# Kernel optimization log

Measured on AMD Instinct MI355X. Metric: run time of the kernel, lower is better.

## Reference

```python
import jax, jax.numpy as jnp
import numpy as np

V = 32000   # vocab_size
E = 400     # EMBEDDING_SIZE
H = 1150    # HIDDEN_SIZE
B = 16      # batch
T = 128     # seq len

# Reference corresponds to model.eval(): LockedDropout and WeightDrop (DropConnect)
# are identity at eval time, so the math is a plain 3-layer LSTM stack with tied
# embedding/output weights. PyTorch LSTM gate order: i, f, g, o.

def _lstm_layer(x_seq, W_ih, W_hh, b_ih, b_hh, hidden):
    # x_seq: (T, B, I); W_ih: (4H', I); W_hh: (4H', H'); biases: (4H',)
    pre = jnp.einsum('tbi,gi->tbg', x_seq, W_ih) + (b_ih + b_hh)  # (T,B,4H')
    h0 = jnp.zeros((x_seq.shape[1], hidden), x_seq.dtype)
    c0 = jnp.zeros_like(h0)

    def step(carry, pre_t):
        h, c = carry
        gates = pre_t + h @ W_hh.T               # (B, 4H')
        i, f, g, o = jnp.split(gates, 4, axis=-1)
        i = jax.nn.sigmoid(i); f = jax.nn.sigmoid(f)
        g = jnp.tanh(g);       o = jax.nn.sigmoid(o)
        c = f * c + i * g
        h = o * jnp.tanh(c)
        return (h, c), h

    (h_T, c_T), ys = jax.lax.scan(step, (h0, c0), pre)
    return ys, h_T, c_T  # ys: (T,B,H')


def setup_inputs() -> dict:
    key = jax.random.key(0)
    ks = jax.random.split(key, 16)
    s = 1.0 / np.sqrt(H)
    u = lambda k, shape: jax.random.uniform(k, shape, jnp.float32, -s, s)
    inp = {
        'emb':   jax.random.uniform(ks[0], (V, E), jnp.float32, -0.1, 0.1),
        'W_ih1': u(ks[1], (4 * H, E)),  'W_hh1': u(ks[2], (4 * H, H)),
        'b_ih1': u(ks[3], (4 * H,)),    'b_hh1': u(ks[4], (4 * H,)),
        'W_ih2': u(ks[5], (4 * H, H)),  'W_hh2': u(ks[6], (4 * H, H)),
        'b_ih2': u(ks[7], (4 * H,)),    'b_hh2': u(ks[8], (4 * H,)),
        'W_ih3': u(ks[9], (4 * E, H)),  'W_hh3': u(ks[10], (4 * E, E)),
        'b_ih3': u(ks[11], (4 * E,)),   'b_hh3': u(ks[12], (4 * E,)),
        'lin_b': u(ks[13], (V,)),
        'x': jax.random.randint(ks[14], (B, T), 0, V, jnp.int32),
    }
    return inp


def reference(emb, W_ih1, W_hh1, b_ih1, b_hh1,
              W_ih2, W_hh2, b_ih2, b_hh2,
              W_ih3, W_hh3, b_ih3, b_hh3,
              lin_b, x):
    xe = emb[x]                       # (B,T,E)
    xs = jnp.transpose(xe, (1, 0, 2)) # (T,B,E)
    xs, h1, c1 = _lstm_layer(xs, W_ih1, W_hh1, b_ih1, b_hh1, H)
    xs, h2, c2 = _lstm_layer(xs, W_ih2, W_hh2, b_ih2, b_hh2, H)
    xs, h3, c3 = _lstm_layer(xs, W_ih3, W_hh3, b_ih3, b_hh3, E)
    xb = jnp.transpose(xs, (1, 0, 2))                 # (B,T,E)
    logits = jnp.einsum('bte,ve->btv', xb, emb) + lin_b  # tied weights
    out = jnp.transpose(logits, (0, 2, 1))            # (B,V,T)
    return out, h1, h2, h3, c1, c2, c3
```

## Files before the change

kernel.cpp:

```cpp
#include <hip/hip_runtime.h>

typedef _Float16 f16;
typedef _Float16 f16x8 __attribute__((ext_vector_type(8)));
typedef float f32x4 __attribute__((ext_vector_type(4)));

#define BB 16
#define TT 128
#define VV 32000
#define EE 400
#define HH 1150
#define MM 2048

#define NWG1 144
#define NWG2 144
#define NWG3 52
#define NSTEPS 130

__device__ __forceinline__ float sigm(float x){ return 1.f/(1.f + __expf(-x)); }
__device__ __forceinline__ float ftanh(float x){ return 2.f/(1.f + __expf(-2.f*x)) - 1.f; }

__device__ __forceinline__ void ld16c(f16x8& d, const f16* p){
    asm volatile("global_load_dwordx4 %0, %1, off sc0 sc1"
                 : "=v"(d) : "v"(p) : "memory");
}
__device__ __forceinline__ void st2c(f16* p, f16 v){
    asm volatile("global_store_short %0, %1, off sc0 sc1"
                 :: "v"(p), "v"(v) : "memory");
}


__global__ void conv_emb(const float* __restrict__ src, f16* __restrict__ dst){
    int v = blockIdx.y;
    int k = blockIdx.x*256 + threadIdx.x;
    if (k >= 416) return;
    float val = (k < EE) ? src[v*EE + k] : 0.f;
    dst[v*416 + k] = (f16)val;
}

__global__ void embed_gather(const float* __restrict__ emb, const int* __restrict__ x,
                             f16* __restrict__ dst){
    int m = blockIdx.y;
    int k = blockIdx.x*256 + threadIdx.x;
    if (k >= 416) return;
    int t = m >> 4, b = m & 15;
    int row = x[b*TT + t];
    float val = (k < EE) ? emb[row*EE + k] : 0.f;
    dst[m*416 + k] = (f16)val;
}

__global__ void conv_w(const float* __restrict__ src, f16* __restrict__ dst,
                       int Hout, int Ksrc, int Kp){
    int n = blockIdx.y;
    int k = blockIdx.x*256 + threadIdx.x;
    if (k >= Kp) return;
    int j = n >> 2, g = n & 3;
    float val = (j < Hout && k < Ksrc) ? src[(g*Hout + j)*Ksrc + k] : 0.f;
    dst[(size_t)n*Kp + k] = (f16)val;
}

__global__ void conv_bias(const float* __restrict__ bi, const float* __restrict__ bh,
                          float* __restrict__ dst, int Hout, int Np){
    int n = blockIdx.x*256 + threadIdx.x;
    if (n >= Np) return;
    int j = n >> 2, g = n & 3;
    dst[n] = (j < Hout) ? (bi[g*Hout + j] + bh[g*Hout + j]) : 0.f;
}

template<int SC>
__global__ __launch_bounds__(256) void gemm16(
    const f16* __restrict__ A, const f16* __restrict__ B,
    const float* __restrict__ bias, float* __restrict__ C,
    int Kp, int Nst)
{
    __shared__ __align__(16) f16 lA[128*32];
    __shared__ __align__(16) f16 lB[128*32];
    const int lane = threadIdx.x & 63;
    const int wid  = threadIdx.x >> 6;
    const int m0 = blockIdx.y * 128, n0 = blockIdx.x * 128;
    f32x4 acc[4][4] = {};
    const int sr = threadIdx.x >> 2;
    const int sc = (threadIdx.x & 3) * 8;
    for (int k0 = 0; k0 < Kp; k0 += 32) {
        __syncthreads();
        *(f16x8*)&lA[ sr      *32 + sc] = *(const f16x8*)&A[(size_t)(m0 + sr     )*Kp + k0 + sc];
        *(f16x8*)&lA[(sr + 64)*32 + sc] = *(const f16x8*)&A[(size_t)(m0 + sr + 64)*Kp + k0 + sc];
        *(f16x8*)&lB[ sr      *32 + sc] = *(const f16x8*)&B[(size_t)(n0 + sr     )*Kp + k0 + sc];
        *(f16x8*)&lB[(sr + 64)*32 + sc] = *(const f16x8*)&B[(size_t)(n0 + sr + 64)*Kp + k0 + sc];
        __syncthreads();
        const int wr = (wid >> 1) * 64, wc = (wid & 1) * 64;
        f16x8 af[4], bf[4];
        #pragma unroll
        for (int i = 0; i < 4; ++i)
            af[i] = *(const f16x8*)&lA[(wr + i*16 + (lane & 15))*32 + (lane >> 4)*8];
        #pragma unroll
        for (int j = 0; j < 4; ++j)
            bf[j] = *(const f16x8*)&lB[(wc + j*16 + (lane & 15))*32 + (lane >> 4)*8];
        #pragma unroll
        for (int i = 0; i < 4; ++i)
            #pragma unroll
            for (int j = 0; j < 4; ++j)
                acc[i][j] = __builtin_amdgcn_mfma_f32_16x16x32_f16(af[i], bf[j], acc[i][j], 0, 0, 0);
    }
    const int wr = (wid >> 1) * 64, wc = (wid & 1) * 64;
    #pragma unroll
    for (int i = 0; i < 4; ++i) {
        #pragma unroll
        for (int j = 0; j < 4; ++j) {
            int gc = n0 + wc + j*16 + (lane & 15);
            float bb = bias[gc];
            #pragma unroll
            for (int r = 0; r < 4; ++r) {
                int gr = m0 + wr + i*16 + (lane >> 4)*4 + r;
                float v = acc[i][j][r] + bb;
                if (SC) C[((size_t)(gr >> 7)*VV + gc)*TT + (gr & 127)] = v;
                else    C[(size_t)gr*Nst + gc] = v;
            }
        }
    }
}


template<int KIH, int KHH, int DELAY>
__device__ __forceinline__ void lstm_role(
    float (&red)[4][16][32], float (&cst)[16][8],
    const float* __restrict__ pre,
    const float* __restrict__ bias,
    const f16* __restrict__ Wih,
    const f16* __restrict__ Whh,
    const f16* __restrict__ xA, const f16* __restrict__ xB,
    f16* __restrict__ hA, f16* __restrict__ hB,
    f16* __restrict__ xs3,
    float* __restrict__ hout, float* __restrict__ cout,
    unsigned* __restrict__ arrive, int bid, int H)
{
    constexpr int HpHH = KHH * 128;
    constexpr int KIHA = (KIH > 0) ? KIH : 1;
    const int lane = threadIdx.x & 63, kw = threadIdx.x >> 6;
    const int n0 = bid * 32;
    const int nwg = gridDim.x;
    if (threadIdx.x < 128) cst[threadIdx.x & 15][threadIdx.x >> 4] = 0.f;
    const int arow = lane & 15, aoff = (lane >> 4) * 8;
    const size_t hofsHH = (size_t)arow * HpHH + kw * (KHH * 32) + aoff;
    const size_t hofsIH = (size_t)arow * 1152 + kw * 288 + aoff;

    const f16* wph0 = Whh + (size_t)(n0 + arow) * HpHH + kw * (KHH * 32) + aoff;
    const f16* wph1 = wph0 + (size_t)16 * HpHH;
    const f16* wpi0 = (KIH > 0) ? (Wih + (size_t)(n0 + arow) * 1152 + kw * 288 + aoff) : nullptr;
    const f16* wpi1 = (KIH > 0) ? (wpi0 + (size_t)16 * 1152) : nullptr;
    f16x8 wh0[KHH], wh1[KHH];
    #pragma unroll
    for (int i = 0; i < KHH; ++i) {
        wh0[i] = *(const f16x8*)(wph0 + i*32);
        wh1[i] = *(const f16x8*)(wph1 + i*32);
    }
    f16x8 wi0[KIHA], wi1[KIHA];
    if constexpr (KIH > 0) {
        #pragma unroll
        for (int i = 0; i < KIH; ++i) {
            wi0[i] = *(const f16x8*)(wpi0 + i*32);
            wi1[i] = *(const f16x8*)(wpi1 + i*32);
        }
    }
    const int b  = threadIdx.x & 15;
    const int jl = threadIdx.x >> 4;
    f32x4 bias4 = {0.f,0.f,0.f,0.f};
    if constexpr (KIH > 0) {
        if (threadIdx.x < 128) bias4 = *(const f32x4*)(bias + n0 + jl*4);
    }
    __syncthreads();

    for (int s = 0; s < NSTEPS; ++s) {
        const int t = s - DELAY;
        if (t >= 0 && t < TT) {
            const f16* hp = ((t & 1) ? hB : hA) + hofsHH;
            f16* hw       =  (t & 1) ? hA : hB;
            f32x4 p4;
            if constexpr (KIH == 0) {
                if (threadIdx.x < 128)
                    p4 = *(const f32x4*)(pre + (size_t)(t*16 + b)*4608 + n0 + jl*4);
            }
            f16x8 xv[KIHA], hv[KHH];
            if constexpr (KIH > 0) {
                const f16* xp = ((t & 1) ? xA : xB) + hofsIH;
                #pragma unroll
                for (int i = 0; i < KIH; ++i) ld16c(xv[i], xp + i*32);
            }
            #pragma unroll
            for (int i = 0; i < KHH; ++i) ld16c(hv[i], hp + i*32);
            asm volatile("s_waitcnt vmcnt(0)" ::: "memory");
            __builtin_amdgcn_sched_barrier(0);

            f32x4 acc0 = {0.f,0.f,0.f,0.f}, acc1 = {0.f,0.f,0.f,0.f};
            if constexpr (KIH > 0) {
                #pragma unroll
                for (int i = 0; i < KIH; ++i) {
                    acc0 = __builtin_amdgcn_mfma_f32_16x16x32_f16(xv[i], wi0[i], acc0, 0, 0, 0);
                    acc1 = __builtin_amdgcn_mfma_f32_16x16x32_f16(xv[i], wi1[i], acc1, 0, 0, 0);
                }
            }
            #pragma unroll
            for (int i = 0; i < KHH; ++i) {
                acc0 = __builtin_amdgcn_mfma_f32_16x16x32_f16(hv[i], wh0[i], acc0, 0, 0, 0);
                acc1 = __builtin_amdgcn_mfma_f32_16x16x32_f16(hv[i], wh1[i], acc1, 0, 0, 0);
            }
            #pragma unroll
            for (int r = 0; r < 4; ++r) {
                red[kw][(lane >> 4)*4 + r][lane & 15]        = acc0[r];
                red[kw][(lane >> 4)*4 + r][16 + (lane & 15)] = acc1[r];
            }
            __syncthreads();
            if (threadIdx.x < 128) {
                const int nb = jl * 4;
                f32x4 base = (KIH > 0) ? bias4 : p4;
                float gi = base[0] + red[0][b][nb+0] + red[1][b][nb+0] + red[2][b][nb+0] + red[3][b][nb+0];
                float gf = base[1] + red[0][b][nb+1] + red[1][b][nb+1] + red[2][b][nb+1] + red[3][b][nb+1];
                float gg = base[2] + red[0][b][nb+2] + red[1][b][nb+2] + red[2][b][nb+2] + red[3][b][nb+2];
                float go = base[3] + red[0][b][nb+3] + red[1][b][nb+3] + red[2][b][nb+3] + red[3][b][nb+3];
                float c = sigm(gf) * cst[b][jl] + sigm(gi) * ftanh(gg);
                float h = sigm(go) * ftanh(c);
                cst[b][jl] = c;
                const int j = (n0 >> 2) + jl;
                st2c(hw + b*HpHH + j, (f16)h);
                if constexpr (DELAY == 2) xs3[(size_t)(b*TT + t)*416 + j] = (f16)h;
                if (t == TT-1 && j < H) { hout[b*H + j] = h; cout[b*H + j] = c; }
                asm volatile("s_waitcnt vmcnt(0)" ::: "memory");
            }
        }
        if (s == NSTEPS-1) break;
        __syncthreads();
        if (threadIdx.x == 0)
            __hip_atomic_store(&arrive[blockIdx.x * 16], (unsigned)(s + 1),
                               __ATOMIC_RELAXED, __HIP_MEMORY_SCOPE_AGENT);
        for (int w = threadIdx.x; w < nwg; w += 256) {
            while (__hip_atomic_load(&arrive[w * 16], __ATOMIC_RELAXED,
                                     __HIP_MEMORY_SCOPE_AGENT) < (unsigned)(s + 1))
                __builtin_amdgcn_s_sleep(1);
        }
        __syncthreads();
    }
}

__global__ __launch_bounds__(256, 2) void lstm_mega(
    const float* __restrict__ pre1,
    const float* __restrict__ bias2, const float* __restrict__ bias3,
    const f16* __restrict__ whh1,
    const f16* __restrict__ wih2, const f16* __restrict__ whh2,
    const f16* __restrict__ wih3, const f16* __restrict__ whh3,
    f16* h1A, f16* h1B, f16* h2A, f16* h2B, f16* h3A, f16* h3B,
    f16* xs3,
    float* h1o, float* c1o, float* h2o, float* c2o, float* h3o, float* c3o,
    unsigned* arrive)
{
    __shared__ float red[4][16][32];
    __shared__ float cst[16][8];
    const int bx = blockIdx.x;
    if (bx < NWG1) {
        lstm_role<0,9,0>(red, cst, pre1, nullptr, nullptr, whh1,
                         nullptr, nullptr, h1A, h1B, nullptr,
                         h1o, c1o, arrive, bx, HH);
    } else if (bx < NWG1 + NWG2) {
        lstm_role<9,9,1>(red, cst, nullptr, bias2, wih2, whh2,
                         h1A, h1B, h2A, h2B, nullptr,
                         h2o, c2o, arrive, bx - NWG1, HH);
    } else {
        lstm_role<9,4,2>(red, cst, nullptr, bias3, wih3, whh3,
                         h2A, h2B, h3A, h3B, xs3,
                         h3o, c3o, arrive, bx - NWG1 - NWG2, EE);
    }
}

extern "C" void kernel_launch(void* const* d_in, const int* in_sizes, int n_in,
                              void* d_out, int out_size, void* d_ws, size_t ws_size,
                              hipStream_t stream)
{
    const float* emb  = (const float*)d_in[0];
    const float* Wih1 = (const float*)d_in[1];
    const float* Whh1 = (const float*)d_in[2];
    const float* bih1 = (const float*)d_in[3];
    const float* bhh1 = (const float*)d_in[4];
    const float* Wih2 = (const float*)d_in[5];
    const float* Whh2 = (const float*)d_in[6];
    const float* bih2 = (const float*)d_in[7];
    const float* bhh2 = (const float*)d_in[8];
    const float* Wih3 = (const float*)d_in[9];
    const float* Whh3 = (const float*)d_in[10];
    const float* bih3 = (const float*)d_in[11];
    const float* bhh3 = (const float*)d_in[12];
    const float* linb = (const float*)d_in[13];
    const int*   x    = (const int*)d_in[14];
    float* out = (float*)d_out;
    char*  ws  = (char*)d_ws;
    char*  outc = (char*)d_out;

    const size_t ARR  = 0;
    const size_t H1A  = 21760;
    const size_t H1B  = H1A + 36864;
    const size_t H2A  = H1B + 36864;
    const size_t H2B  = H2A + 36864;
    const size_t H3A  = H2B + 36864;
    const size_t H3B  = H3A + 16384;
    const size_t ZEND = H3B + 16384;
    size_t off = ZEND;
    auto alloc = [&](size_t bytes){ size_t r = off; off += (bytes + 255) & ~(size_t)255; return r; };
    const size_t EMBBF = alloc((size_t)VV*416*2);
    const size_t XS0   = alloc((size_t)MM*416*2);
    const size_t XS3   = alloc((size_t)MM*416*2);
    const size_t WIH1  = alloc((size_t)4608*416*2);
    const size_t B1    = alloc((size_t)4608*4);
    const size_t B2    = alloc((size_t)4608*4);
    const size_t B3    = alloc((size_t)1664*4);

    f16* emb_bf = (f16*)(ws + EMBBF);
    f16* xs0    = (f16*)(ws + XS0);
    f16* xs3    = (f16*)(ws + XS3);
    f16* wih1p  = (f16*)(ws + WIH1);
    float* bias1 = (float*)(ws + B1);
    float* bias2 = (float*)(ws + B2);
    float* bias3 = (float*)(ws + B3);
    unsigned* arr = (unsigned*)(ws + ARR);

    float* pre1 = out;
    const size_t OW_HH1 = 37748736;
    const size_t OW_IH2 = OW_HH1 + 10616832;
    const size_t OW_HH2 = OW_IH2 + 10616832;
    const size_t OW_IH3 = OW_HH2 + 10616832;
    const size_t OW_HH3 = OW_IH3 + 3833856;
    f16* whh1p = (f16*)(outc + OW_HH1);
    f16* wih2p = (f16*)(outc + OW_IH2);
    f16* whh2p = (f16*)(outc + OW_HH2);
    f16* wih3p = (f16*)(outc + OW_IH3);
    f16* whh3p = (f16*)(outc + OW_HH3);

    float* H1O = out + 65536000;  float* H2O = H1O + 18400;  float* H3O = H2O + 18400;
    float* C1O = H3O + 6400;      float* C2O = C1O + 18400;  float* C3O = C2O + 18400;

    hipMemsetAsync(d_ws, 0, ZEND, stream);

    conv_emb    <<<dim3(2, VV), 256, 0, stream>>>(emb, emb_bf);
    embed_gather<<<dim3(2, MM), 256, 0, stream>>>(emb, x, xs0);

    conv_w   <<<dim3(2, 4608), 256, 0, stream>>>(Wih1, wih1p, HH, EE, 416);
    conv_bias<<<dim3(18),      256, 0, stream>>>(bih1, bhh1, bias1, HH, 4608);
    gemm16<0><<<dim3(36, 16),  256, 0, stream>>>(xs0, wih1p, bias1, pre1, 416, 4608);

    conv_w   <<<dim3(5, 4608), 256, 0, stream>>>(Whh1, whh1p, HH, HH, 1152);
    conv_w   <<<dim3(5, 4608), 256, 0, stream>>>(Wih2, wih2p, HH, HH, 1152);
    conv_w   <<<dim3(5, 4608), 256, 0, stream>>>(Whh2, whh2p, HH, HH, 1152);
    conv_w   <<<dim3(5, 1664), 256, 0, stream>>>(Wih3, wih3p, EE, HH, 1152);
    conv_w   <<<dim3(2, 1664), 256, 0, stream>>>(Whh3, whh3p, EE, EE, 512);
    conv_bias<<<dim3(18),      256, 0, stream>>>(bih2, bhh2, bias2, HH, 4608);
    conv_bias<<<dim3(7),       256, 0, stream>>>(bih3, bhh3, bias3, EE, 1664);

    lstm_mega<<<dim3(NWG1 + NWG2 + NWG3), 256, 0, stream>>>(
        pre1, bias2, bias3, whh1p, wih2p, whh2p, wih3p, whh3p,
        (f16*)(ws+H1A), (f16*)(ws+H1B), (f16*)(ws+H2A), (f16*)(ws+H2B),
        (f16*)(ws+H3A), (f16*)(ws+H3B),
        xs3, H1O, C1O, H2O, C2O, H3O, C3O, arr);

    gemm16<1><<<dim3(250, 16), 256, 0, stream>>>(xs3, emb_bf, linb, out, 416, 0);
}
```

Before: 1.336 ms.

## Give layer-1 and layer-3 LSTM workgroups four gate groups and halve grid

```diff
diff --git a/kernel.cpp b/kernel.cpp
--- a/kernel.cpp
+++ b/kernel.cpp
@@ -11,9 +11,10 @@
 #define HH 1150
 #define MM 2048
 
-#define NWG1 144
+#define NWG1 72
 #define NWG2 144
-#define NWG3 52
+#define NWG3 26
+#define NWGT (NWG1+NWG2+NWG3)
 #define NSTEPS 130
 
 __device__ __forceinline__ float sigm(float x){ return 1.f/(1.f + __expf(-x)); }
@@ -120,9 +121,9 @@
 }
 
 
-template<int KIH, int KHH, int DELAY>
+template<int KIH, int KHH, int DELAY, int NG>
 __device__ __forceinline__ void lstm_role(
-    float (&red)[4][16][32], float (&cst)[16][8],
+    float (&red)[4][16][66], float (&cst)[16][16],
     const float* __restrict__ pre,
     const float* __restrict__ bias,
     const f16* __restrict__ Wih,
@@ -135,37 +136,36 @@
 {
     constexpr int HpHH = KHH * 128;
     constexpr int KIHA = (KIH > 0) ? KIH : 1;
+    constexpr int G = NG * 16;
     const int lane = threadIdx.x & 63, kw = threadIdx.x >> 6;
-    const int n0 = bid * 32;
+    const int n0 = bid * G;
     const int nwg = gridDim.x;
-    if (threadIdx.x < 128) cst[threadIdx.x & 15][threadIdx.x >> 4] = 0.f;
+    cst[threadIdx.x & 15][threadIdx.x >> 4] = 0.f;
     const int arow = lane & 15, aoff = (lane >> 4) * 8;
     const size_t hofsHH = (size_t)arow * HpHH + kw * (KHH * 32) + aoff;
     const size_t hofsIH = (size_t)arow * 1152 + kw * 288 + aoff;
 
-    const f16* wph0 = Whh + (size_t)(n0 + arow) * HpHH + kw * (KHH * 32) + aoff;
-    const f16* wph1 = wph0 + (size_t)16 * HpHH;
-    const f16* wpi0 = (KIH > 0) ? (Wih + (size_t)(n0 + arow) * 1152 + kw * 288 + aoff) : nullptr;
-    const f16* wpi1 = (KIH > 0) ? (wpi0 + (size_t)16 * 1152) : nullptr;
-    f16x8 wh0[KHH], wh1[KHH];
+    f16x8 wh[NG][KHH];
     #pragma unroll
-    for (int i = 0; i < KHH; ++i) {
-        wh0[i] = *(const f16x8*)(wph0 + i*32);
-        wh1[i] = *(const f16x8*)(wph1 + i*32);
-    }
-    f16x8 wi0[KIHA], wi1[KIHA];
+    for (int g = 0; g < NG; ++g) {
+        const f16* wp = Whh + (size_t)(n0 + g*16 + arow) * HpHH + kw * (KHH*32) + aoff;
+        #pragma unroll
+        for (int i = 0; i < KHH; ++i) wh[g][i] = *(const f16x8*)(wp + i*32);
+    }
+    f16x8 wi[NG][KIHA];
     if constexpr (KIH > 0) {
         #pragma unroll
-        for (int i = 0; i < KIH; ++i) {
-            wi0[i] = *(const f16x8*)(wpi0 + i*32);
-            wi1[i] = *(const f16x8*)(wpi1 + i*32);
+        for (int g = 0; g < NG; ++g) {
+            const f16* wp = Wih + (size_t)(n0 + g*16 + arow) * 1152 + kw * 288 + aoff;
+            #pragma unroll
+            for (int i = 0; i < KIH; ++i) wi[g][i] = *(const f16x8*)(wp + i*32);
         }
     }
     const int b  = threadIdx.x & 15;
     const int jl = threadIdx.x >> 4;
     f32x4 bias4 = {0.f,0.f,0.f,0.f};
     if constexpr (KIH > 0) {
-        if (threadIdx.x < 128) bias4 = *(const f32x4*)(bias + n0 + jl*4);
+        if (threadIdx.x < NG*64) bias4 = *(const f32x4*)(bias + n0 + jl*4);
     }
     __syncthreads();
 
@@ -176,7 +176,7 @@
             f16* hw       =  (t & 1) ? hA : hB;
             f32x4 p4;
             if constexpr (KIH == 0) {
-                if (threadIdx.x < 128)
+                if (threadIdx.x < NG*64)
                     p4 = *(const f32x4*)(pre + (size_t)(t*16 + b)*4608 + n0 + jl*4);
             }
             f16x8 xv[KIHA], hv[KHH];
@@ -190,26 +190,27 @@
             asm volatile("s_waitcnt vmcnt(0)" ::: "memory");
             __builtin_amdgcn_sched_barrier(0);
 
-            f32x4 acc0 = {0.f,0.f,0.f,0.f}, acc1 = {0.f,0.f,0.f,0.f};
+            f32x4 acc[NG] = {};
             if constexpr (KIH > 0) {
                 #pragma unroll
-                for (int i = 0; i < KIH; ++i) {
-                    acc0 = __builtin_amdgcn_mfma_f32_16x16x32_f16(xv[i], wi0[i], acc0, 0, 0, 0);
-                    acc1 = __builtin_amdgcn_mfma_f32_16x16x32_f16(xv[i], wi1[i], acc1, 0, 0, 0);
-                }
-            }
-            #pragma unroll
-            for (int i = 0; i < KHH; ++i) {
-                acc0 = __builtin_amdgcn_mfma_f32_16x16x32_f16(hv[i], wh0[i], acc0, 0, 0, 0);
-                acc1 = __builtin_amdgcn_mfma_f32_16x16x32_f16(hv[i], wh1[i], acc1, 0, 0, 0);
-            }
-            #pragma unroll
-            for (int r = 0; r < 4; ++r) {
-                red[kw][(lane >> 4)*4 + r][lane & 15]        = acc0[r];
-                red[kw][(lane >> 4)*4 + r][16 + (lane & 15)] = acc1[r];
-            }
+                for (int i = 0; i < KIH; ++i)
+                    #pragma unroll
+                    for (int g = 0; g < NG; ++g)
+                        acc[g] = __builtin_amdgcn_mfma_f32_16x16x32_f16(xv[i], wi[g][i], acc[g], 0, 0, 0);
+            }
+            #pragma unroll
+            for (int i = 0; i < KHH; ++i)
+                #pragma unroll
+                for (int g = 0; g < NG; ++g)
+                    acc[g] = __builtin_amdgcn_mfma_f32_16x16x32_f16(hv[i], wh[g][i], acc[g], 0, 0, 0);
+
+            #pragma unroll
+            for (int g = 0; g < NG; ++g)
+                #pragma unroll
+                for (int r = 0; r < 4; ++r)
+                    red[kw][(lane >> 4)*4 + r][g*16 + (lane & 15)] = acc[g][r];
             __syncthreads();
-            if (threadIdx.x < 128) {
+            if (threadIdx.x < NG*64) {
                 const int nb = jl * 4;
                 f32x4 base = (KIH > 0) ? bias4 : p4;
                 float gi = base[0] + red[0][b][nb+0] + red[1][b][nb+0] + red[2][b][nb+0] + red[3][b][nb+0];
@@ -240,7 +241,7 @@
     }
 }
 
-__global__ __launch_bounds__(256, 2) void lstm_mega(
+__global__ __launch_bounds__(256, 1) void lstm_mega(
     const float* __restrict__ pre1,
     const float* __restrict__ bias2, const float* __restrict__ bias3,
     const f16* __restrict__ whh1,
@@ -251,21 +252,21 @@
     float* h1o, float* c1o, float* h2o, float* c2o, float* h3o, float* c3o,
     unsigned* arrive)
 {
-    __shared__ float red[4][16][32];
-    __shared__ float cst[16][8];
+    __shared__ float red[4][16][66];
+    __shared__ float cst[16][16];
     const int bx = blockIdx.x;
     if (bx < NWG1) {
-        lstm_role<0,9,0>(red, cst, pre1, nullptr, nullptr, whh1,
-                         nullptr, nullptr, h1A, h1B, nullptr,
-                         h1o, c1o, arrive, bx, HH);
+        lstm_role<0,9,0,4>(red, cst, pre1, nullptr, nullptr, whh1,
+                           nullptr, nullptr, h1A, h1B, nullptr,
+                           h1o, c1o, arrive, bx, HH);
     } else if (bx < NWG1 + NWG2) {
-        lstm_role<9,9,1>(red, cst, nullptr, bias2, wih2, whh2,
-                         h1A, h1B, h2A, h2B, nullptr,
-                         h2o, c2o, arrive, bx - NWG1, HH);
+        lstm_role<9,9,1,2>(red, cst, nullptr, bias2, wih2, whh2,
+                           h1A, h1B, h2A, h2B, nullptr,
+                           h2o, c2o, arrive, bx - NWG1, HH);
     } else {
-        lstm_role<9,4,2>(red, cst, nullptr, bias3, wih3, whh3,
-                         h2A, h2B, h3A, h3B, xs3,
-                         h3o, c3o, arrive, bx - NWG1 - NWG2, EE);
+        lstm_role<9,4,2,4>(red, cst, nullptr, bias3, wih3, whh3,
+                           h2A, h2B, h3A, h3B, xs3,
+                           h3o, c3o, arrive, bx - NWG1 - NWG2, EE);
     }
 }
 
@@ -351,7 +352,7 @@
     conv_bias<<<dim3(18),      256, 0, stream>>>(bih2, bhh2, bias2, HH, 4608);
     conv_bias<<<dim3(7),       256, 0, stream>>>(bih3, bhh3, bias3, EE, 1664);
 
-    lstm_mega<<<dim3(NWG1 + NWG2 + NWG3), 256, 0, stream>>>(
+    lstm_mega<<<dim3(NWGT), 256, 0, stream>>>(
         pre1, bias2, bias3, whh1p, wih2p, whh2p, wih3p, whh3p,
         (f16*)(ws+H1A), (f16*)(ws+H1B), (f16*)(ws+H2A), (f16*)(ws+H2B),
         (f16*)(ws+H3A), (f16*)(ws+H3B),
```

Result: faster. 1.196 ms (-10.5%).
